# Kernel optimization log

Measured on AMD Instinct MI355X. Metric: run time of the kernel, lower is better.

## Reference

```python
import jax, jax.numpy as jnp
import numpy as np

N_BUSES = 2000
W1, W2, W3, LMBDA = 1.0, 1.0, 1.0, 0.1


def setup_inputs() -> dict:
    key = jax.random.key(0)
    k0, k1, k2, k3, k4 = jax.random.split(key, 5)
    B, E = 32, 6000
    x = jax.random.normal(k0, (B * N_BUSES, 6), jnp.float32)
    edge_attr = jax.random.normal(k1, (B * E, 2), jnp.float32)
    edge_index = jax.random.randint(k2, (2, B * E), 0, N_BUSES)
    outputs = jax.random.normal(k3, (B * N_BUSES, 2), jnp.float32)
    labels = jax.random.normal(k4, (B * N_BUSES, 2), jnp.float32)
    return {"x": x, "edge_attr": edge_attr, "edge_index": edge_index,
            "outputs": outputs, "labels": labels}


def _physics_terms(x, edge_attr, edge_index, outputs):
    B = x.shape[0] // N_BUSES
    # Vpred: complex voltage prediction, (B, N, 1)
    Vpred = (outputs[:, 0] + 1j * outputs[:, 1]).astype(jnp.complex64)
    Vpred = Vpred.reshape(B, N_BUSES, 1)
    nf = x.reshape(B, N_BUSES, 6)
    ea = edge_attr.reshape(B, -1, 2)
    E = ea.shape[1]
    ei = edge_index.reshape(2, B, E) % N_BUSES  # (2, B, E)
    S = (nf[:, :, 0] + 1j * nf[:, :, 1]).astype(jnp.complex64)  # (B, N)
    Vm = nf[:, :, 2]
    bus_type = nf[:, :, 3:6]
    adm = (ea[:, :, 0] + 1j * ea[:, :, 1]).astype(jnp.complex64)  # (B, E)
    # scatter edge admittances into dense Y (B, N, N)
    b_idx = jnp.arange(B)[:, None]
    Y = jnp.zeros((B, N_BUSES, N_BUSES), jnp.complex64)
    Y = Y.at[b_idx, ei[0], ei[1]].set(adm)
    # Spred = V * conj(Y @ V)
    YV = jnp.matmul(Y, Vpred)                      # (B, N, 1)
    Spred = (Vpred * jnp.conj(YV))[:, :, 0]        # (B, N)
    S_mean = jnp.mean(S, axis=1, keepdims=True)
    S_inverse = jnp.where(S != 0, 1.0 / S, 1.0 / S_mean)
    S_inverse_norm = jnp.abs(S_inverse)
    result1 = ((Spred - S) ** 2) * bus_type[:, :, 0]                    # complex
    result2 = ((Spred.real - S.real) ** 2) * bus_type[:, :, 1]          # real
    Vm_mean = jnp.mean(Vm, axis=1, keepdims=True)
    Vm_inverse = jnp.where(Vm != 0, 1.0 / Vm, 1.0 / Vm_mean)
    D1 = S_inverse_norm * (result1 + result2)                           # complex
    Vmag = jnp.abs(Vpred[:, :, 0])
    D2 = jnp.abs(Vmag * (bus_type[:, :, 1] + bus_type[:, :, 2]) - Vm) * Vm_inverse
    D3 = jnp.abs(Vpred[:, :, 0].imag * bus_type[:, :, 2]) * Vm_inverse
    return jnp.mean(D1), jnp.mean(D2), jnp.mean(D3)


def reference(x, edge_attr, edge_index, outputs, labels):
    d1, d2, d3 = _physics_terms(x, edge_attr, edge_index, outputs)
    physics_loss = W1 * d1 + W2 * d2 + W3 * d3  # complex (D1 is complex, as in torch)
    mse = jnp.mean((outputs - labels) ** 2)
    loss = mse + LMBDA * physics_loss
    return loss, physics_loss, d1, d2, d3
```

## Files before the change

kernel.cpp:

```cpp
#include <hip/hip_runtime.h>

typedef unsigned long long ull;

#define N_BUSES     2000
#define BATCH       32
#define EDGES_PER_B 6000
#define TOTAL_BUSES (BATCH * N_BUSES)
#define TOTAL_EDGES (BATCH * EDGES_PER_B)

#define SPLIT   8
#define BUS_PER (N_BUSES / SPLIT)
#define TPB     1024
#define NBLOCKS (BATCH * SPLIT)
#define EPT     6

#define HBITS 11
#define HSIZE (1 << HBITS)
#define HMASK (HSIZE - 1)

__device__ __forceinline__ unsigned hash_key(int key) {
    return ((unsigned)key * 2654435761u) >> (32 - HBITS);
}

__global__ __launch_bounds__(TPB)
void fused_split(const float* __restrict__ x, const float* __restrict__ ea,
                 const int* __restrict__ ei, const float* __restrict__ outputs,
                 const float* __restrict__ labels, double* __restrict__ part) {
    __shared__ ull slots[HSIZE];
    __shared__ float yv_sh[2 * BUS_PER];
    __shared__ double red[5][TPB / 64];
    __shared__ double red2[3][TPB / 64];
    __shared__ float bst[3];
    __shared__ int pend[64];
    __shared__ int npend;

    const int blk = blockIdx.x;
    const int b = blk / SPLIT;
    const int p = blk % SPLIT;
    const int r0 = p * BUS_PER;
    const int tid = threadIdx.x;
    const int wave = tid >> 6, lane = tid & 63;

    float2 q0, q1, q2, vP, lP;
    const int idxP = b * N_BUSES + r0 + tid;
    if (tid < BUS_PER) {
        const float2* row2 = (const float2*)(x + (size_t)idxP * 6);
        q0 = row2[0]; q1 = row2[1]; q2 = row2[2];
        vP = ((const float2*)outputs)[idxP];
        lP = ((const float2*)labels)[idxP];
    }

    int iv[EPT], jv[EPT];
#pragma unroll
    for (int k = 0; k < EPT; k++) {
        int e = tid + k * TPB;
        if (e < EDGES_PER_B) {
            iv[k] = ei[b * EDGES_PER_B + e] % N_BUSES;
            jv[k] = ei[TOTAL_EDGES + b * EDGES_PER_B + e] % N_BUSES;
        } else { iv[k] = -1; jv[k] = 0; }
    }
    float2 av[EPT], vv[EPT];
    bool inr[EPT];
#pragma unroll
    for (int k = 0; k < EPT; k++) {
        int i = iv[k];
        inr[k] = (i >= r0) && (i < r0 + BUS_PER);
        if (inr[k]) {
            av[k] = ((const float2*)ea)[b * EDGES_PER_B + tid + k * TPB];
            vv[k] = ((const float2*)outputs)[b * N_BUSES + jv[k]];
        }
    }

    slots[tid] = 0ULL;
    slots[tid + TPB] = 0ULL;
    if (tid < 2 * BUS_PER) yv_sh[tid] = 0.0f;
    if (tid == 0) npend = 0;
    __syncthreads();

#pragma unroll
    for (int k = 0; k < EPT; k++) {
        if (!inr[k]) continue;
        int e = tid + k * TPB;
        int i = iv[k], j = jv[k];
        int key = i * N_BUSES + j;
        ull tag = (ull)(unsigned)(key + 1) << 13;
        ull packed = tag | (unsigned)e;
        unsigned h = hash_key(key);
        int deposed = -1;
        bool we_add = false;
        while (true) {
            ull old = atomicCAS(&slots[h], 0ULL, packed);
            if (old == 0ULL) { we_add = true; break; }
            if ((old >> 13) == (ull)(unsigned)(key + 1)) {
                ull prev = atomicMax(&slots[h], packed);
                if (prev < packed) { we_add = true; deposed = (int)(prev & 0x1FFFULL); }
                break;
            }
            h = (h + 1) & HMASK;
        }
        if (we_add) {
            float2 a = av[k], v = vv[k];
            float addr = a.x * v.x - a.y * v.y;
            float addi = a.x * v.y + a.y * v.x;
            if (deposed >= 0) {
                float2 ap = ((const float2*)ea)[b * EDGES_PER_B + deposed];
                addr -= ap.x * v.x - ap.y * v.y;
                addi -= ap.x * v.y + ap.y * v.x;
            }
            int il = i - r0;
            atomicAdd(&yv_sh[2 * il],     addr);
            atomicAdd(&yv_sh[2 * il + 1], addi);
        }
    }
    __syncthreads();

    double t0 = 0.0, t1 = 0.0, t2 = 0.0, t3 = 0.0, t4 = 0.0;
    if (tid < BUS_PER) {
        int il = tid;
        float sre = q0.x, sim = q0.y, Vm = q1.x;
        float bt0 = q1.y, bt1 = q2.x, bt2 = q2.y;
        if ((sre == 0.0f && sim == 0.0f) || Vm == 0.0f) {
            int pp = atomicAdd(&npend, 1);
            if (pp < 64) pend[pp] = il;
        } else {
            float yvr = yv_sh[2 * il], yvi = yv_sh[2 * il + 1];
            float spr = vP.x * yvr + vP.y * yvi;
            float spi = vP.y * yvr - vP.x * yvi;
            float den = sre * sre + sim * sim;
            float ir = sre / den, ii = -sim / den;
            float sinv_norm = sqrtf(ir * ir + ii * ii);
            float cr = spr - sre, ci = spi - sim;
            t0 = (double)(sinv_norm * ((cr * cr - ci * ci) * bt0 + (cr * cr) * bt1));
            t1 = (double)(sinv_norm * (2.0f * cr * ci * bt0));
            float vminv = 1.0f / Vm;
            float vmag = sqrtf(vP.x * vP.x + vP.y * vP.y);
            t2 = (double)(fabsf(vmag * (bt1 + bt2) - Vm) * vminv);
            t3 = (double)(fabsf(vP.y * bt2) * vminv);
            float e0 = vP.x - lP.x, e1 = vP.y - lP.y;
            t4 = (double)(e0 * e0 + e1 * e1);
        }
    }
    for (int off = 32; off > 0; off >>= 1) {
        t0 += __shfl_down(t0, off, 64);
        t1 += __shfl_down(t1, off, 64);
        t2 += __shfl_down(t2, off, 64);
        t3 += __shfl_down(t3, off, 64);
        t4 += __shfl_down(t4, off, 64);
    }
    if (lane == 0) {
        red[0][wave] = t0; red[1][wave] = t1; red[2][wave] = t2;
        red[3][wave] = t3; red[4][wave] = t4;
    }
    __syncthreads();

    double a0 = 0, a1 = 0, a2 = 0, a3 = 0, a4 = 0;
    if (tid == 0) {
        for (int w = 0; w < TPB / 64; w++) {
            a0 += red[0][w]; a1 += red[1][w]; a2 += red[2][w];
            a3 += red[3][w]; a4 += red[4][w];
        }
    }

    if (npend > 0) {
        double sre = 0.0, sim = 0.0, svm = 0.0;
        for (int i = tid; i < N_BUSES; i += TPB) {
            const float* row = x + (size_t)(b * N_BUSES + i) * 6;
            sre += (double)row[0];
            sim += (double)row[1];
            svm += (double)row[2];
        }
        for (int off = 32; off > 0; off >>= 1) {
            sre += __shfl_down(sre, off, 64);
            sim += __shfl_down(sim, off, 64);
            svm += __shfl_down(svm, off, 64);
        }
        if (lane == 0) { red2[0][wave] = sre; red2[1][wave] = sim; red2[2][wave] = svm; }
        __syncthreads();
        if (tid == 0) {
            double sa = 0, sb = 0, sc = 0;
            for (int w = 0; w < TPB / 64; w++) { sa += red2[0][w]; sb += red2[1][w]; sc += red2[2][w]; }
            bst[0] = (float)(sa / N_BUSES);
            bst[1] = (float)(sb / N_BUSES);
            bst[2] = (float)(sc / N_BUSES);
        }
        __syncthreads();
        if (tid == 0) {
            int np = npend < 64 ? npend : 64;
            for (int q = 0; q < np; q++) {
                int il = pend[q];
                int idx = b * N_BUSES + r0 + il;
                const float2* row2 = (const float2*)(x + (size_t)idx * 6);
                float2 w0 = row2[0], w1 = row2[1], w2 = row2[2];
                float sr = w0.x, si = w0.y, Vm = w1.x;
                float bt0 = w1.y, bt1 = w2.x, bt2 = w2.y;
                float2 v = ((const float2*)outputs)[idx];
                float yvr = yv_sh[2 * il], yvi = yv_sh[2 * il + 1];
                float spr = v.x * yvr + v.y * yvi;
                float spi = v.y * yvr - v.x * yvi;
                float ir, ii;
                if (sr != 0.0f || si != 0.0f) {
                    float den = sr * sr + si * si;
                    ir = sr / den; ii = -si / den;
                } else {
                    float mr = bst[0], mi = bst[1];
                    float den = mr * mr + mi * mi;
                    ir = mr / den; ii = -mi / den;
                }
                float sinv_norm = sqrtf(ir * ir + ii * ii);
                float cr = spr - sr, ci = spi - si;
                a0 += (double)(sinv_norm * ((cr * cr - ci * ci) * bt0 + (cr * cr) * bt1));
                a1 += (double)(sinv_norm * (2.0f * cr * ci * bt0));
                float vminv = (Vm != 0.0f) ? (1.0f / Vm) : (1.0f / bst[2]);
                float vmag = sqrtf(v.x * v.x + v.y * v.y);
                a2 += (double)(fabsf(vmag * (bt1 + bt2) - Vm) * vminv);
                a3 += (double)(fabsf(v.y * bt2) * vminv);
                float2 l = ((const float2*)labels)[idx];
                float e0 = v.x - l.x, e1 = v.y - l.y;
                a4 += (double)(e0 * e0 + e1 * e1);
            }
        }
    }

    if (tid == 0) {
        part[blk * 5 + 0] = a0; part[blk * 5 + 1] = a1; part[blk * 5 + 2] = a2;
        part[blk * 5 + 3] = a3; part[blk * 5 + 4] = a4;
    }
}

__global__ __launch_bounds__(256)
void finalize(const double* __restrict__ part, float* __restrict__ out, int out_size) {
    int tid = threadIdx.x;
    int wave = tid >> 6, lane = tid & 63;
    double v0 = part[tid * 5 + 0], v1 = part[tid * 5 + 1], v2 = part[tid * 5 + 2];
    double v3 = part[tid * 5 + 3], v4 = part[tid * 5 + 4];
    for (int off = 32; off > 0; off >>= 1) {
        v0 += __shfl_down(v0, off, 64);
        v1 += __shfl_down(v1, off, 64);
        v2 += __shfl_down(v2, off, 64);
        v3 += __shfl_down(v3, off, 64);
        v4 += __shfl_down(v4, off, 64);
    }
    __shared__ double sh[5][4];
    if (lane == 0) {
        sh[0][wave] = v0; sh[1][wave] = v1; sh[2][wave] = v2;
        sh[3][wave] = v3; sh[4][wave] = v4;
    }
    __syncthreads();
    if (tid == 0) {
        double a0 = 0, a1 = 0, a2 = 0, a3 = 0, a4 = 0;
        for (int w = 0; w < 4; w++) {
            a0 += sh[0][w]; a1 += sh[1][w]; a2 += sh[2][w];
            a3 += sh[3][w]; a4 += sh[4][w];
        }
        double inv = 1.0 / (double)TOTAL_BUSES;
        double d1re = a0 * inv, d1im = a1 * inv;
        double d2 = a2 * inv, d3 = a3 * inv;
        double mse = a4 / (2.0 * (double)TOTAL_BUSES);
        double phre = d1re + d2 + d3, phim = d1im;
        double lre = mse + 0.1 * phre, lim = 0.1 * phim;
        if (out_size == 8) {
            out[0] = (float)lre;  out[1] = (float)lim;
            out[2] = (float)phre; out[3] = (float)phim;
            out[4] = (float)d1re; out[5] = (float)d1im;
            out[6] = (float)d2;   out[7] = (float)d3;
        } else {
            float vals[5] = {(float)lre, (float)phre, (float)d1re, (float)d2, (float)d3};
            int n = out_size < 5 ? out_size : 5;
            for (int k = 0; k < n; k++) out[k] = vals[k];
            for (int k = 5; k < out_size && k < 64; k++) out[k] = 0.0f;
        }
    }
}

extern "C" void kernel_launch(void* const* d_in, const int* in_sizes, int n_in,
                              void* d_out, int out_size, void* d_ws, size_t ws_size,
                              hipStream_t stream) {
    const float* x       = (const float*)d_in[0];
    const float* ea      = (const float*)d_in[1];
    const int*   ei      = (const int*)d_in[2];
    const float* outputs = (const float*)d_in[3];
    const float* labels  = (const float*)d_in[4];
    double* part = (double*)d_ws;

    fused_split<<<NBLOCKS, TPB, 0, stream>>>(x, ea, ei, outputs, labels, part);
    finalize<<<1, 256, 0, stream>>>(part, (float*)d_out, out_size);
}
```

Before: 83.61 us.

## Merge finalize into main kernel via cooperative grid sync; vectorize edge loads

Replaces the separate finalize launch with a grid-wide cooperative sync, after which block 0 reduces the per-block partials. This removes one kernel launch and its gap. Edge indices are now assigned contiguously per thread, six per thread, and loaded as int2 vectors, so fewer threads carry edge work. The grid sync adds barrier cost, the partial writes and reads use atomics to make them visible across blocks, and the cooperative launch needs all 256 blocks of 1024 threads resident at the same time.

```diff
diff --git a/kernel.cpp b/kernel.cpp
--- a/kernel.cpp
+++ b/kernel.cpp
@@ -1,5 +1,7 @@
 #include <hip/hip_runtime.h>
-
+#include <hip/hip_cooperative_groups.h>
+
+namespace cg = cooperative_groups;
 typedef unsigned long long ull;
 
 #define N_BUSES     2000
@@ -22,10 +24,11 @@
     return ((unsigned)key * 2654435761u) >> (32 - HBITS);
 }
 
-__global__ __launch_bounds__(TPB)
-void fused_split(const float* __restrict__ x, const float* __restrict__ ea,
-                 const int* __restrict__ ei, const float* __restrict__ outputs,
-                 const float* __restrict__ labels, double* __restrict__ part) {
+__global__ __launch_bounds__(TPB, 4)
+void fused_all(const float* __restrict__ x, const float* __restrict__ ea,
+               const int* __restrict__ ei, const float* __restrict__ outputs,
+               const float* __restrict__ labels, double* __restrict__ part,
+               float* __restrict__ out, int out_size) {
     __shared__ ull slots[HSIZE];
     __shared__ float yv_sh[2 * BUS_PER];
     __shared__ double red[5][TPB / 64];
@@ -50,23 +53,25 @@
         lP = ((const float2*)labels)[idxP];
     }
 
+    const bool act = tid < (EDGES_PER_B / EPT);
     int iv[EPT], jv[EPT];
-#pragma unroll
-    for (int k = 0; k < EPT; k++) {
-        int e = tid + k * TPB;
-        if (e < EDGES_PER_B) {
-            iv[k] = ei[b * EDGES_PER_B + e] % N_BUSES;
-            jv[k] = ei[TOTAL_EDGES + b * EDGES_PER_B + e] % N_BUSES;
-        } else { iv[k] = -1; jv[k] = 0; }
+    if (act) {
+        const int* pi = ei + (size_t)b * EDGES_PER_B + tid * EPT;
+        int2 a0 = *(const int2*)pi, a1 = *(const int2*)(pi + 2), a2 = *(const int2*)(pi + 4);
+        const int* pj = pi + TOTAL_EDGES;
+        int2 c0 = *(const int2*)pj, c1 = *(const int2*)(pj + 2), c2 = *(const int2*)(pj + 4);
+        iv[0] = a0.x % N_BUSES; iv[1] = a0.y % N_BUSES; iv[2] = a1.x % N_BUSES;
+        iv[3] = a1.y % N_BUSES; iv[4] = a2.x % N_BUSES; iv[5] = a2.y % N_BUSES;
+        jv[0] = c0.x % N_BUSES; jv[1] = c0.y % N_BUSES; jv[2] = c1.x % N_BUSES;
+        jv[3] = c1.y % N_BUSES; jv[4] = c2.x % N_BUSES; jv[5] = c2.y % N_BUSES;
     }
     float2 av[EPT], vv[EPT];
     bool inr[EPT];
 #pragma unroll
     for (int k = 0; k < EPT; k++) {
-        int i = iv[k];
-        inr[k] = (i >= r0) && (i < r0 + BUS_PER);
+        inr[k] = act && (iv[k] >= r0) && (iv[k] < r0 + BUS_PER);
         if (inr[k]) {
-            av[k] = ((const float2*)ea)[b * EDGES_PER_B + tid + k * TPB];
+            av[k] = ((const float2*)ea)[b * EDGES_PER_B + tid * EPT + k];
             vv[k] = ((const float2*)outputs)[b * N_BUSES + jv[k]];
         }
     }
@@ -80,7 +85,7 @@
 #pragma unroll
     for (int k = 0; k < EPT; k++) {
         if (!inr[k]) continue;
-        int e = tid + k * TPB;
+        int e = tid * EPT + k;
         int i = iv[k], j = jv[k];
         int key = i * N_BUSES + j;
         ull tag = (ull)(unsigned)(key + 1) << 13;
@@ -222,17 +227,23 @@
     }
 
     if (tid == 0) {
-        part[blk * 5 + 0] = a0; part[blk * 5 + 1] = a1; part[blk * 5 + 2] = a2;
-        part[blk * 5 + 3] = a3; part[blk * 5 + 4] = a4;
-    }
-}
-
-__global__ __launch_bounds__(256)
-void finalize(const double* __restrict__ part, float* __restrict__ out, int out_size) {
-    int tid = threadIdx.x;
-    int wave = tid >> 6, lane = tid & 63;
-    double v0 = part[tid * 5 + 0], v1 = part[tid * 5 + 1], v2 = part[tid * 5 + 2];
-    double v3 = part[tid * 5 + 3], v4 = part[tid * 5 + 4];
+        atomicExch((ull*)&part[blk * 5 + 0], __double_as_longlong(a0));
+        atomicExch((ull*)&part[blk * 5 + 1], __double_as_longlong(a1));
+        atomicExch((ull*)&part[blk * 5 + 2], __double_as_longlong(a2));
+        atomicExch((ull*)&part[blk * 5 + 3], __double_as_longlong(a3));
+        atomicExch((ull*)&part[blk * 5 + 4], __double_as_longlong(a4));
+    }
+    cg::this_grid().sync();
+
+    if (blk != 0) return;
+    double v0 = 0, v1 = 0, v2 = 0, v3 = 0, v4 = 0;
+    if (tid < NBLOCKS) {
+        v0 = atomicAdd(&part[tid * 5 + 0], 0.0);
+        v1 = atomicAdd(&part[tid * 5 + 1], 0.0);
+        v2 = atomicAdd(&part[tid * 5 + 2], 0.0);
+        v3 = atomicAdd(&part[tid * 5 + 3], 0.0);
+        v4 = atomicAdd(&part[tid * 5 + 4], 0.0);
+    }
     for (int off = 32; off > 0; off >>= 1) {
         v0 += __shfl_down(v0, off, 64);
         v1 += __shfl_down(v1, off, 64);
@@ -240,22 +251,22 @@
         v3 += __shfl_down(v3, off, 64);
         v4 += __shfl_down(v4, off, 64);
     }
-    __shared__ double sh[5][4];
-    if (lane == 0) {
-        sh[0][wave] = v0; sh[1][wave] = v1; sh[2][wave] = v2;
-        sh[3][wave] = v3; sh[4][wave] = v4;
+    __syncthreads();
+    if (lane == 0 && tid < NBLOCKS) {
+        red[0][wave] = v0; red[1][wave] = v1; red[2][wave] = v2;
+        red[3][wave] = v3; red[4][wave] = v4;
     }
     __syncthreads();
     if (tid == 0) {
-        double a0 = 0, a1 = 0, a2 = 0, a3 = 0, a4 = 0;
-        for (int w = 0; w < 4; w++) {
-            a0 += sh[0][w]; a1 += sh[1][w]; a2 += sh[2][w];
-            a3 += sh[3][w]; a4 += sh[4][w];
+        double s0 = 0, s1 = 0, s2 = 0, s3 = 0, s4 = 0;
+        for (int w = 0; w < NBLOCKS / 64; w++) {
+            s0 += red[0][w]; s1 += red[1][w]; s2 += red[2][w];
+            s3 += red[3][w]; s4 += red[4][w];
         }
         double inv = 1.0 / (double)TOTAL_BUSES;
-        double d1re = a0 * inv, d1im = a1 * inv;
-        double d2 = a2 * inv, d3 = a3 * inv;
-        double mse = a4 / (2.0 * (double)TOTAL_BUSES);
+        double d1re = s0 * inv, d1im = s1 * inv;
+        double d2 = s2 * inv, d3 = s3 * inv;
+        double mse = s4 / (2.0 * (double)TOTAL_BUSES);
         double phre = d1re + d2 + d3, phim = d1im;
         double lre = mse + 0.1 * phre, lim = 0.1 * phim;
         if (out_size == 8) {
@@ -281,7 +292,10 @@
     const float* outputs = (const float*)d_in[3];
     const float* labels  = (const float*)d_in[4];
     double* part = (double*)d_ws;
-
-    fused_split<<<NBLOCKS, TPB, 0, stream>>>(x, ea, ei, outputs, labels, part);
-    finalize<<<1, 256, 0, stream>>>(part, (float*)d_out, out_size);
+    float* outp = (float*)d_out;
+
+    void* args[] = {(void*)&x, (void*)&ea, (void*)&ei, (void*)&outputs,
+                    (void*)&labels, (void*)&part, (void*)&outp, (void*)&out_size};
+    hipLaunchCooperativeKernel((const void*)fused_all, dim3(NBLOCKS), dim3(TPB),
+                               args, 0, stream);
 }
```

After: 122.6 us. 46.6% more time.
